# Optimization experiments

Hardware: AMD Instinct MI355X
Metric: run time of the kernel (lower is better)

Reference implementation:

```python
import jax, jax.numpy as jnp
import numpy as np

B, L, DIM, H = 2, 2048, 1024, 16
HD = DIM // H  # 64
EPS = 1e-6
ROPE_THETA = 10000.0


def _rmsnorm(x, scale):
    # mean of squares in float32 as in torch (dtype=torch.float32)
    ms = jnp.mean(jnp.square(x.astype(jnp.float32)), axis=-1, keepdims=True)
    inv = jax.lax.rsqrt(ms + EPS).astype(x.dtype)
    return x * inv * scale.astype(x.dtype)


def _rope_cos_sin(seq_len, head_dim, dtype):
    inv_freq = 1.0 / (ROPE_THETA ** (jnp.arange(0, head_dim, 2, dtype=jnp.float32) / head_dim))
    ang = jnp.arange(seq_len, dtype=jnp.float32)[:, None] * inv_freq[None, :]  # [L, HD/2]
    cos = jnp.cos(ang)[:, None, :].astype(dtype)  # [L,1,HD/2] broadcast over heads
    sin = jnp.sin(ang)[:, None, :].astype(dtype)
    return cos, sin


def _rope_apply(x, cos, sin):
    # x: [B,L,H,HD]; rotate-half formulation
    x1, x2 = jnp.split(x, 2, axis=-1)
    return jnp.concatenate([x1 * cos - x2 * sin, x2 * cos + x1 * sin], axis=-1)


def setup_inputs() -> dict:
    key = jax.random.key(0)
    k1, k2, k3 = jax.random.split(key, 3)
    x = jax.random.normal(k1, (B, L, DIM), dtype=jnp.float32)
    Wqkv = jax.random.normal(k2, (DIM, 3 * DIM), dtype=jnp.float32) * (DIM ** -0.5)
    Wproj = jax.random.normal(k3, (DIM, DIM), dtype=jnp.float32) * (DIM ** -0.5)
    q_scale = jnp.ones((HD,), dtype=jnp.float32)
    k_scale = jnp.ones((HD,), dtype=jnp.float32)
    bproj = jnp.zeros((DIM,), dtype=jnp.float32)
    return {"x": x, "Wqkv": Wqkv, "q_scale": q_scale, "k_scale": k_scale,
            "Wproj": Wproj, "bproj": bproj}


def reference(x, Wqkv, q_scale, k_scale, Wproj, bproj):
    b, l, c = x.shape
    qkv = x @ Wqkv  # [B,L,3*DIM]
    qkv = qkv.reshape(b, l, 3, H, HD)
    q, k, v = qkv[:, :, 0], qkv[:, :, 1], qkv[:, :, 2]  # each [B,L,H,HD]
    q = _rmsnorm(q, q_scale)
    k = _rmsnorm(k, k_scale)
    cos, sin = _rope_cos_sin(l, HD, x.dtype)
    q = _rope_apply(q, cos, sin)
    k = _rope_apply(k, cos, sin)
    scale = HD ** -0.5
    scores = jnp.einsum('blhd,bmhd->bhlm', q, k) * scale  # [B,H,L,L]
    p = jax.nn.softmax(scores, axis=-1)
    o = jnp.einsum('bhlm,bmhd->blhd', p, v).reshape(b, l, c)
    return o @ Wproj + bproj
```

## Files before the change

### kernel.cpp

```cpp
#include <hip/hip_runtime.h>
#include <hip/hip_bf16.h>
#include <cstdint>

#define B_   2
#define L_   2048
#define DIM_ 1024
#define H_   16
#define HD_  64
#define M_   (B_ * L_)
#define N3_  (3 * DIM_)

typedef unsigned short ushort_t;
typedef __bf16 bf16x8 __attribute__((ext_vector_type(8)));
typedef float  f32x4  __attribute__((ext_vector_type(4)));
typedef float  f32x16 __attribute__((ext_vector_type(16)));
typedef unsigned u32x2_t __attribute__((ext_vector_type(2)));

__device__ __forceinline__ unsigned short f2b(float f) {
  return __builtin_bit_cast(unsigned short, (__bf16)f);
}
__device__ __forceinline__ float b2f(unsigned short s) {
  unsigned u = ((unsigned)s) << 16;
  return __builtin_bit_cast(float, u);
}
__device__ __forceinline__ float fmax3(float a, float b, float c) {
  return fmaxf(fmaxf(a, b), c);
}

__device__ __forceinline__ void plswap(unsigned &a, unsigned &b) {
#if defined(__has_builtin) && __has_builtin(__builtin_amdgcn_permlane32_swap)
  u32x2_t r = __builtin_amdgcn_permlane32_swap(a, b, false, false);
  a = r[0]; b = r[1];
#else
  unsigned sa = (unsigned)__shfl_xor((int)a, 32);
  unsigned sb = (unsigned)__shfl_xor((int)b, 32);
  bool hi = (threadIdx.x & 32) != 0;
  unsigned na = hi ? sb : a;
  unsigned nb = hi ? b : sa;
  a = na; b = nb;
#endif
}

typedef const __attribute__((address_space(1))) void* as1cp;
typedef __attribute__((address_space(3))) void* as3p;
__device__ __forceinline__ void gload_lds16(const void* g, void* l) {
  __builtin_amdgcn_global_load_lds((as1cp)g, (as3p)l, 16, 0, 0);
}

__global__ __launch_bounds__(256)
void conv_bf16(const float* __restrict__ in, ushort_t* __restrict__ out, int n4) {
  int i = blockIdx.x * 256 + threadIdx.x;
  if (i >= n4) return;
  float4 v = *(const float4*)&in[(size_t)i * 4];
  ushort4 o;
  o.x = f2b(v.x); o.y = f2b(v.y); o.z = f2b(v.z); o.w = f2b(v.w);
  *(ushort4*)&out[(size_t)i * 4] = o;
}

__global__ __launch_bounds__(256)
void transpose_conv(const float* __restrict__ in, ushort_t* __restrict__ out,
                    int R, int C) {
  __shared__ float tile[64][65];
  const int t = threadIdx.x;
  const int r0 = blockIdx.y * 64, c0 = blockIdx.x * 64;
#pragma unroll
  for (int p = 0; p < 4; ++p) {
    int r = (t >> 4) + p * 16;
    int c = (t & 15) * 4;
    float4 v = *(const float4*)&in[(size_t)(r0 + r) * C + (c0 + c)];
    tile[r][c + 0] = v.x; tile[r][c + 1] = v.y;
    tile[r][c + 2] = v.z; tile[r][c + 3] = v.w;
  }
  __syncthreads();
#pragma unroll
  for (int p = 0; p < 4; ++p) {
    int cc = (t >> 4) + p * 16;
    int r  = (t & 15) * 4;
    ushort4 o;
    o.x = f2b(tile[r + 0][cc]); o.y = f2b(tile[r + 1][cc]);
    o.z = f2b(tile[r + 2][cc]); o.w = f2b(tile[r + 3][cc]);
    *(ushort4*)&out[(size_t)(c0 + cc) * R + (r0 + r)] = o;
  }
}

__global__ __launch_bounds__(256)
void rope_tab(float* __restrict__ cosT, float* __restrict__ sinT) {
  int idx = blockIdx.x * 256 + threadIdx.x;
  int l = idx >> 5, d = idx & 31;
  float inv_freq = expf(-((float)(2 * d) / 64.f) * logf(10000.f));
  float ang = (float)l * inv_freq;
  cosT[idx] = cosf(ang);
  sinT[idx] = sinf(ang);
}

template <int MODE>
__global__ __launch_bounds__(256)
void gemm_bt(const ushort_t* __restrict__ A, const ushort_t* __restrict__ BT,
             void* __restrict__ Cout, ushort_t* __restrict__ vtout,
             const float* __restrict__ bias, int M, int N, int K, int ldc) {
  __shared__ ushort_t As[128 * 32];
  __shared__ ushort_t Bs[128 * 32];
  const int lane = threadIdx.x & 63;
  const int wid  = threadIdx.x >> 6;
  const int wm = wid >> 1, wn = wid & 1;
  const int m0 = blockIdx.y * 128, n0 = blockIdx.x * 128;
  const int ro = lane & 15, kg = lane >> 4;

  f32x4 acc[4][4] = {};

  for (int k0 = 0; k0 < K; k0 += 32) {
    const int cb = wid * 128;
#pragma unroll
    for (int j = 0; j < 2; ++j) {
      int c = cb + j * 64 + lane;
      gload_lds16(A + (size_t)(m0 + (c >> 2)) * K + k0 + (c & 3) * 8,
                  &As[(cb + j * 64) * 8]);
    }
#pragma unroll
    for (int j = 0; j < 2; ++j) {
      int c = cb + j * 64 + lane;
      gload_lds16(BT + (size_t)(n0 + (c >> 2)) * K + k0 + (c & 3) * 8,
                  &Bs[(cb + j * 64) * 8]);
    }
    __syncthreads();
    bf16x8 af[4], bfr[4];
#pragma unroll
    for (int i = 0; i < 4; ++i)
      af[i] = *(const bf16x8*)&As[(wm * 64 + i * 16 + ro) * 32 + kg * 8];
#pragma unroll
    for (int i = 0; i < 4; ++i)
      bfr[i] = *(const bf16x8*)&Bs[(wn * 64 + i * 16 + ro) * 32 + kg * 8];
#pragma unroll
    for (int i = 0; i < 4; ++i)
#pragma unroll
      for (int j = 0; j < 4; ++j)
        acc[i][j] = __builtin_amdgcn_mfma_f32_16x16x32_bf16(af[i], bfr[j],
                                                            acc[i][j], 0, 0, 0);
    __syncthreads();
  }

  if (MODE == 0) {
    if (n0 < 2048) {
#pragma unroll
      for (int i = 0; i < 4; ++i)
#pragma unroll
        for (int r = 0; r < 4; ++r) {
          int row = m0 + wm * 64 + i * 16 + kg * 4 + r;
#pragma unroll
          for (int j = 0; j < 4; ++j) {
            int col = n0 + wn * 64 + j * 16 + ro;
            ((ushort_t*)Cout)[(size_t)row * ldc + col] = f2b(acc[i][j][r]);
          }
        }
    } else {
#pragma unroll
      for (int i = 0; i < 4; ++i) {
        int rowb = m0 + wm * 64 + i * 16 + kg * 4;
        int bb = rowb >> 11, l = rowb & (L_ - 1);
#pragma unroll
        for (int j = 0; j < 4; ++j) {
          int dg = (n0 - 2048) + wn * 64 + j * 16 + ro;
          ushort4 o;
          o.x = f2b(acc[i][j][0]); o.y = f2b(acc[i][j][1]);
          o.z = f2b(acc[i][j][2]); o.w = f2b(acc[i][j][3]);
          *(ushort4*)&vtout[((size_t)bb * DIM_ + dg) * L_ + l] = o;
        }
      }
    }
  } else {
#pragma unroll
    for (int i = 0; i < 4; ++i)
#pragma unroll
      for (int r = 0; r < 4; ++r) {
        int row = m0 + wm * 64 + i * 16 + kg * 4 + r;
#pragma unroll
        for (int j = 0; j < 4; ++j) {
          int col = n0 + wn * 64 + j * 16 + ro;
          ((float*)Cout)[(size_t)row * ldc + col] = acc[i][j][r] + bias[col];
        }
      }
  }
}

__global__ __launch_bounds__(256)
void rmsrope(ushort_t* __restrict__ qk, const float* __restrict__ qs,
             const float* __restrict__ ks, const float* __restrict__ cosT,
             const float* __restrict__ sinT) {
  const int t = blockIdx.x;
  const int l = t & (L_ - 1);
  const int j = threadIdx.x & 15;
  const int h = threadIdx.x >> 4;
  const int dd = (j & 7) * 4;
  float4 cv = *(const float4*)&cosT[l * 32 + dd];
  float4 sv = *(const float4*)&sinT[l * 32 + dd];
  const float sgn = (j < 8) ? -1.f : 1.f;
#pragma unroll
  for (int ic = 0; ic < 2; ++ic) {
    const float qsc = (ic == 0) ? 0.125f * 1.44269504088896341f : 1.f;
    ushort_t* base = qk + (size_t)t * 2048 + ic * DIM_ + h * HD_ + j * 4;
    ushort4 raw = *(const ushort4*)base;
    float x0 = b2f(raw.x), x1 = b2f(raw.y), x2 = b2f(raw.z), x3 = b2f(raw.w);
    float ss = x0 * x0 + x1 * x1 + x2 * x2 + x3 * x3;
    ss += __shfl_xor(ss, 1); ss += __shfl_xor(ss, 2);
    ss += __shfl_xor(ss, 4); ss += __shfl_xor(ss, 8);
    float inv = rsqrtf(ss * (1.f / 64.f) + 1e-6f);
    const float* scp = (ic == 0 ? qs : ks) + j * 4;
    float4 sc = *(const float4*)scp;
    x0 *= inv * sc.x; x1 *= inv * sc.y; x2 *= inv * sc.z; x3 *= inv * sc.w;
    float y0 = __shfl_xor(x0, 8), y1 = __shfl_xor(x1, 8);
    float y2 = __shfl_xor(x2, 8), y3 = __shfl_xor(x3, 8);
    ushort4 o;
    o.x = f2b((x0 * cv.x + sgn * y0 * sv.x) * qsc);
    o.y = f2b((x1 * cv.y + sgn * y1 * sv.y) * qsc);
    o.z = f2b((x2 * cv.z + sgn * y2 * sv.z) * qsc);
    o.w = f2b((x3 * cv.w + sgn * y3 * sv.w) * qsc);
    *(ushort4*)base = o;
  }
}

template <int SPLIT>
__global__ __launch_bounds__(256, 3)
void flash_attn(const ushort_t* __restrict__ qk, const ushort_t* __restrict__ vt,
                ushort_t* __restrict__ O, ushort_t* __restrict__ Opart,
                float* __restrict__ Ml) {
  const int qt = blockIdx.x, h = blockIdx.y;
  const int b  = SPLIT ? (int)(blockIdx.z >> 1) : (int)blockIdx.z;
  const int ks = SPLIT ? (int)(blockIdx.z & 1) : 0;
  const int ktBeg = SPLIT ? ks * (L_ / 128) : 0;
  const int ktEnd = SPLIT ? ktBeg + (L_ / 128) : (L_ / 64);
  const int lane = threadIdx.x & 63, wid = threadIdx.x >> 6;
  const int lq = lane & 31;
  const int hi = lane >> 5;
  const int q0 = qt * 128;
  const size_t tok0 = (size_t)b * L_;
  const ushort_t* qb = qk + tok0 * 2048 + h * HD_;
  const ushort_t* kb = qb + DIM_;
  const ushort_t* vb = vt + ((size_t)b * DIM_ + h * HD_) * L_;

  __shared__ ushort_t Ks[2][4096];
  __shared__ ushort_t Vs[2][4096];

  const int srow0 = wid * 16 + (lane >> 3);
  const int sc    = (lane & 7) ^ (srow0 & 7);
  const ushort_t* kst = kb + (size_t)(ktBeg * 64 + srow0) * 2048 + sc * 8;
  const ushort_t* vst = vb + (size_t)srow0 * L_ + ktBeg * 64 + sc * 8;
  auto STAGE = [&](int bufi) {
    gload_lds16(kst,            &Ks[bufi][wid * 1024]);
    gload_lds16(kst + 8 * 2048, &Ks[bufi][wid * 1024 + 512]);
    gload_lds16(vst,            &Vs[bufi][wid * 1024]);
    gload_lds16(vst + 8 * L_,   &Vs[bufi][wid * 1024 + 512]);
    kst += 64 * 2048;
    vst += 64;
  };

  bf16x8 qf[4];
  {
    const ushort_t* gp = qb + (size_t)(q0 + wid * 32 + lq) * 2048;
#pragma unroll
    for (int s = 0; s < 4; ++s)
      qf[s] = *(const bf16x8*)(gp + s * 16 + hi * 8);
  }

  int chs[4];
#pragma unroll
  for (int s = 0; s < 4; ++s) chs[s] = ((2 * s + hi) ^ (lq & 7)) * 8;

  f32x16 oaccT[2] = {};
  float mrow = 0.f;
  float lrow = 0.f;

  STAGE(0);
  __syncthreads();

  auto TILE = [&](int bi, bool more) {
    if (more) STAGE(bi ^ 1);
    const ushort_t* kb0 = &Ks[bi][lq * 64];
    const ushort_t* vb0 = &Vs[bi][lq * 64];
#pragma unroll
    for (int t = 0; t < 2; ++t) {
      f32x16 st;
#pragma unroll
      for (int i = 0; i < 16; ++i) st[i] = -mrow;
      __builtin_amdgcn_s_setprio(1);
#pragma unroll
      for (int s = 0; s < 4; ++s) {
        bf16x8 kf = *(const bf16x8*)(kb0 + t * 2048 + chs[s]);
        st = __builtin_amdgcn_mfma_f32_32x32x16_bf16(kf, qf[s], st, 0, 0, 0);
      }
      __builtin_amdgcn_s_setprio(0);

      float m1 = fmax3(st[0],  st[1],  st[2]);
      float m2 = fmax3(st[3],  st[4],  st[5]);
      float m3 = fmax3(st[6],  st[7],  st[8]);
      float m4 = fmax3(st[9],  st[10], st[11]);
      float m5 = fmax3(st[12], st[13], st[14]);
      float n1 = fmax3(m1, m2, st[15]);
      float n2 = fmax3(m3, m4, m5);
      float pm = fmaxf(n1, n2);
      pm = fmaxf(pm, __shfl_xor(pm, 32));

      if (__any(pm > 8.f)) {
        float d = fmaxf(pm, 0.f);
        float alpha = __builtin_amdgcn_exp2f(-d);
        mrow += d;
        lrow *= alpha;
#pragma unroll
        for (int dt = 0; dt < 2; ++dt)
#pragma unroll
          for (int r = 0; r < 16; ++r) oaccT[dt][r] *= alpha;
#pragma unroll
        for (int i = 0; i < 16; ++i) st[i] -= d;
      }

      unsigned pk[8];
      float rs0 = 0.f, rs1 = 0.f;
#pragma unroll
      for (int p = 0; p < 8; ++p) {
        float e0 = __builtin_amdgcn_exp2f(st[2 * p]);
        float e1 = __builtin_amdgcn_exp2f(st[2 * p + 1]);
        rs0 += e0; rs1 += e1;
        pk[p] = (unsigned)f2b(e0) | ((unsigned)f2b(e1) << 16);
      }
      lrow += rs0 + rs1;

      __builtin_amdgcn_s_setprio(1);
#pragma unroll
      for (int blk = 0; blk < 2; ++blk) {
        unsigned w0 = pk[4 * blk + 0], w1 = pk[4 * blk + 1];
        unsigned w2 = pk[4 * blk + 2], w3 = pk[4 * blk + 3];
        plswap(w0, w2);
        plswap(w1, w3);
        uint4 bw; bw.x = w0; bw.y = w1; bw.z = w2; bw.w = w3;
        bf16x8 pf = __builtin_bit_cast(bf16x8, bw);
        const int sg = 2 * t + blk;
#pragma unroll
        for (int dt = 0; dt < 2; ++dt) {
          bf16x8 vf = *(const bf16x8*)(vb0 + dt * 2048 + chs[sg]);
          oaccT[dt] = __builtin_amdgcn_mfma_f32_32x32x16_bf16(vf, pf,
                                                              oaccT[dt], 0, 0, 0);
        }
      }
      __builtin_amdgcn_s_setprio(0);
    }
    __syncthreads();
  };

  const int NT = ktEnd - ktBeg;
  for (int it = 0; it < NT; it += 2) {
    TILE(0, it + 1 < NT);
    TILE(1, it + 2 < NT);
  }

  lrow += __shfl_xor(lrow, 32);
  const float linv = 1.f / lrow;
  const int tok = (int)tok0 + q0 + wid * 32 + lq;
  ushort_t* obp = (SPLIT ? Opart + (size_t)ks * M_ * DIM_ : O)
                  + (size_t)tok * DIM_ + h * HD_;
#pragma unroll
  for (int dt = 0; dt < 2; ++dt)
#pragma unroll
    for (int g4 = 0; g4 < 4; ++g4) {
      int d0 = dt * 32 + g4 * 8 + hi * 4;
      ushort4 o4;
      o4.x = f2b(oaccT[dt][4 * g4 + 0] * linv);
      o4.y = f2b(oaccT[dt][4 * g4 + 1] * linv);
      o4.z = f2b(oaccT[dt][4 * g4 + 2] * linv);
      o4.w = f2b(oaccT[dt][4 * g4 + 3] * linv);
      *(ushort4*)(obp + d0) = o4;
    }
  if (SPLIT && hi == 0) {
    float2 ml; ml.x = mrow; ml.y = lrow;
    *(float2*)&Ml[(((size_t)ks * M_ + tok) * H_ + h) * 2] = ml;
  }
}

__global__ __launch_bounds__(256)
void attn_combine(const ushort_t* __restrict__ Opart, const float* __restrict__ Ml,
                  ushort_t* __restrict__ O) {
  int idx = blockIdx.x * 256 + threadIdx.x;
  int c   = idx & 127;
  int tok = idx >> 7;
  int h   = c >> 3;
  float2 ml0 = *(const float2*)&Ml[(((size_t)0 * M_ + tok) * H_ + h) * 2];
  float2 ml1 = *(const float2*)&Ml[(((size_t)1 * M_ + tok) * H_ + h) * 2];
  float mM = fmaxf(ml0.x, ml1.x);
  float w0 = ml0.y * __builtin_amdgcn_exp2f(ml0.x - mM);
  float w1 = ml1.y * __builtin_amdgcn_exp2f(ml1.x - mM);
  float inv = 1.f / (w0 + w1);
  w0 *= inv; w1 *= inv;
  size_t off = (size_t)tok * DIM_ + c * 8;
  uint4 a = *(const uint4*)&Opart[off];
  uint4 d = *(const uint4*)&Opart[(size_t)M_ * DIM_ + off];
  auto mix = [&](unsigned ua, unsigned ud) -> unsigned {
    float a0 = b2f((unsigned short)(ua & 0xffff)), a1 = b2f((unsigned short)(ua >> 16));
    float d0 = b2f((unsigned short)(ud & 0xffff)), d1 = b2f((unsigned short)(ud >> 16));
    unsigned r0 = f2b(a0 * w0 + d0 * w1), r1 = f2b(a1 * w0 + d1 * w1);
    return r0 | (r1 << 16);
  };
  uint4 o;
  o.x = mix(a.x, d.x); o.y = mix(a.y, d.y);
  o.z = mix(a.z, d.z); o.w = mix(a.w, d.w);
  *(uint4*)&O[off] = o;
}

extern "C" void kernel_launch(void* const* d_in, const int* in_sizes, int n_in,
                              void* d_out, int out_size, void* d_ws, size_t ws_size,
                              hipStream_t stream) {
  const float* x     = (const float*)d_in[0];
  const float* Wqkv  = (const float*)d_in[1];
  const float* qs    = (const float*)d_in[2];
  const float* ks    = (const float*)d_in[3];
  const float* Wproj = (const float*)d_in[4];
  const float* bproj = (const float*)d_in[5];
  float* out = (float*)d_out;

  char* ws = (char*)d_ws;
  ushort_t* xb     = (ushort_t*)(ws);
  ushort_t* WqkvT  = (ushort_t*)(ws + (size_t)(8u << 20));
  ushort_t* WprojT = (ushort_t*)(ws + (size_t)(14u << 20));
  ushort_t* qkb    = (ushort_t*)(ws + (size_t)(16u << 20));
  ushort_t* vtb    = (ushort_t*)(ws + (size_t)(32u << 20));
  float*    cosT   = (float*)(ws + (size_t)(40u << 20));
  float*    sinT   = (float*)(ws + (size_t)(40u << 20) + (256u << 10));
  ushort_t* ob     = (ushort_t*)(ws + (size_t)(41u << 20));
  ushort_t* Opart  = (ushort_t*)(ws + (size_t)(49u << 20));
  float*    Ml     = (float*)(ws + (size_t)(65u << 20));

  conv_bf16<<<4096, 256, 0, stream>>>(x, xb, M_ * DIM_ / 4);
  transpose_conv<<<dim3(48, 16), 256, 0, stream>>>(Wqkv, WqkvT, DIM_, N3_);
  transpose_conv<<<dim3(16, 16), 256, 0, stream>>>(Wproj, WprojT, DIM_, DIM_);
  rope_tab<<<256, 256, 0, stream>>>(cosT, sinT);
  gemm_bt<0><<<dim3(24, 32), 256, 0, stream>>>(xb, WqkvT, qkb, vtb, nullptr,
                                               M_, N3_, DIM_, 2048);
  rmsrope<<<4096, 256, 0, stream>>>(qkb, qs, ks, cosT, sinT);
  if (ws_size >= ((size_t)66u << 20)) {
    flash_attn<1><<<dim3(16, 16, 4), 256, 0, stream>>>(qkb, vtb, nullptr,
                                                       Opart, Ml);
    attn_combine<<<2048, 256, 0, stream>>>(Opart, Ml, ob);
  } else {
    flash_attn<0><<<dim3(16, 16, 2), 256, 0, stream>>>(qkb, vtb, ob,
                                                       nullptr, nullptr);
  }
  gemm_bt<1><<<dim3(8, 32), 256, 0, stream>>>(ob, WprojT, out, nullptr, bproj,
                                              M_, DIM_, DIM_, DIM_);
}
```

Before: 152.7 us.

## Merge preprocessing kernels, batch both score tiles, compute row sums via MFMA

The four preprocessing launches (x conversion, two weight transposes, rope table) become one kernel that dispatches on block index, which removes launch overhead and the gaps between launches. In flash attention, both 32-key sub-tiles are now processed together: their score MFMAs are interleaved, the max and rescale check run once per 64 keys, and the exponentials are computed as one batch. The softmax denominator is now accumulated by an MFMA of a ones vector against the probability fragment instead of scalar adds and a cross-lane shuffle. This adds matrix work per tile and raises register pressure, and the row sum is now taken from the bf16-rounded probabilities.

```diff
diff --git a/kernel.cpp b/kernel.cpp
--- a/kernel.cpp
+++ b/kernel.cpp
@@ -48,49 +48,55 @@
 }
 
 __global__ __launch_bounds__(256)
-void conv_bf16(const float* __restrict__ in, ushort_t* __restrict__ out, int n4) {
-  int i = blockIdx.x * 256 + threadIdx.x;
-  if (i >= n4) return;
-  float4 v = *(const float4*)&in[(size_t)i * 4];
-  ushort4 o;
-  o.x = f2b(v.x); o.y = f2b(v.y); o.z = f2b(v.z); o.w = f2b(v.w);
-  *(ushort4*)&out[(size_t)i * 4] = o;
-}
-
-__global__ __launch_bounds__(256)
-void transpose_conv(const float* __restrict__ in, ushort_t* __restrict__ out,
-                    int R, int C) {
+void preproc(const float* __restrict__ x, ushort_t* __restrict__ xb,
+             const float* __restrict__ Wqkv, ushort_t* __restrict__ WqkvT,
+             const float* __restrict__ Wproj, ushort_t* __restrict__ WprojT,
+             float* __restrict__ cosT, float* __restrict__ sinT) {
   __shared__ float tile[64][65];
+  const int blk = blockIdx.x;
   const int t = threadIdx.x;
-  const int r0 = blockIdx.y * 64, c0 = blockIdx.x * 64;
-#pragma unroll
-  for (int p = 0; p < 4; ++p) {
-    int r = (t >> 4) + p * 16;
-    int c = (t & 15) * 4;
-    float4 v = *(const float4*)&in[(size_t)(r0 + r) * C + (c0 + c)];
-    tile[r][c + 0] = v.x; tile[r][c + 1] = v.y;
-    tile[r][c + 2] = v.z; tile[r][c + 3] = v.w;
-  }
-  __syncthreads();
-#pragma unroll
-  for (int p = 0; p < 4; ++p) {
-    int cc = (t >> 4) + p * 16;
-    int r  = (t & 15) * 4;
+  if (blk < 4096) {
+    int i = blk * 256 + t;
+    float4 v = *(const float4*)&x[(size_t)i * 4];
     ushort4 o;
-    o.x = f2b(tile[r + 0][cc]); o.y = f2b(tile[r + 1][cc]);
-    o.z = f2b(tile[r + 2][cc]); o.w = f2b(tile[r + 3][cc]);
-    *(ushort4*)&out[(size_t)(c0 + cc) * R + (r0 + r)] = o;
-  }
-}
-
-__global__ __launch_bounds__(256)
-void rope_tab(float* __restrict__ cosT, float* __restrict__ sinT) {
-  int idx = blockIdx.x * 256 + threadIdx.x;
-  int l = idx >> 5, d = idx & 31;
-  float inv_freq = expf(-((float)(2 * d) / 64.f) * logf(10000.f));
-  float ang = (float)l * inv_freq;
-  cosT[idx] = cosf(ang);
-  sinT[idx] = sinf(ang);
+    o.x = f2b(v.x); o.y = f2b(v.y); o.z = f2b(v.z); o.w = f2b(v.w);
+    *(ushort4*)&xb[(size_t)i * 4] = o;
+  } else if (blk < 5120) {
+    const float* in;
+    ushort_t* out;
+    int C, bi;
+    if (blk < 4864) { in = Wqkv; out = WqkvT; C = 3072; bi = blk - 4096; }
+    else            { in = Wproj; out = WprojT; C = 1024; bi = blk - 4864; }
+    const int nbx = C >> 6;
+    const int bx = bi % nbx, by = bi / nbx;
+    const int r0 = by * 64, c0 = bx * 64;
+    const int R = 1024;
+#pragma unroll
+    for (int p = 0; p < 4; ++p) {
+      int r = (t >> 4) + p * 16;
+      int c = (t & 15) * 4;
+      float4 v = *(const float4*)&in[(size_t)(r0 + r) * C + (c0 + c)];
+      tile[r][c + 0] = v.x; tile[r][c + 1] = v.y;
+      tile[r][c + 2] = v.z; tile[r][c + 3] = v.w;
+    }
+    __syncthreads();
+#pragma unroll
+    for (int p = 0; p < 4; ++p) {
+      int cc = (t >> 4) + p * 16;
+      int r  = (t & 15) * 4;
+      ushort4 o;
+      o.x = f2b(tile[r + 0][cc]); o.y = f2b(tile[r + 1][cc]);
+      o.z = f2b(tile[r + 2][cc]); o.w = f2b(tile[r + 3][cc]);
+      *(ushort4*)&out[(size_t)(c0 + cc) * R + (r0 + r)] = o;
+    }
+  } else {
+    int idx = (blk - 5120) * 256 + t;
+    int l = idx >> 5, d = idx & 31;
+    float inv_freq = expf(-((float)(2 * d) / 64.f) * logf(10000.f));
+    float ang = (float)l * inv_freq;
+    cosT[idx] = cosf(ang);
+    sinT[idx] = sinf(ang);
+  }
 }
 
 template <int MODE>
@@ -261,13 +267,17 @@
       qf[s] = *(const bf16x8*)(gp + s * 16 + hi * 8);
   }
 
+  bf16x8 onesv;
+#pragma unroll
+  for (int i = 0; i < 8; ++i) onesv[i] = (__bf16)1.0f;
+
   int chs[4];
 #pragma unroll
   for (int s = 0; s < 4; ++s) chs[s] = ((2 * s + hi) ^ (lq & 7)) * 8;
 
   f32x16 oaccT[2] = {};
+  f32x16 laccv = {};
   float mrow = 0.f;
-  float lrow = 0.f;
 
   STAGE(0);
   __syncthreads();
@@ -276,63 +286,77 @@
     if (more) STAGE(bi ^ 1);
     const ushort_t* kb0 = &Ks[bi][lq * 64];
     const ushort_t* vb0 = &Vs[bi][lq * 64];
-#pragma unroll
-    for (int t = 0; t < 2; ++t) {
-      f32x16 st;
-#pragma unroll
-      for (int i = 0; i < 16; ++i) st[i] = -mrow;
-      __builtin_amdgcn_s_setprio(1);
-#pragma unroll
-      for (int s = 0; s < 4; ++s) {
-        bf16x8 kf = *(const bf16x8*)(kb0 + t * 2048 + chs[s]);
-        st = __builtin_amdgcn_mfma_f32_32x32x16_bf16(kf, qf[s], st, 0, 0, 0);
-      }
-      __builtin_amdgcn_s_setprio(0);
-
-      float m1 = fmax3(st[0],  st[1],  st[2]);
-      float m2 = fmax3(st[3],  st[4],  st[5]);
-      float m3 = fmax3(st[6],  st[7],  st[8]);
-      float m4 = fmax3(st[9],  st[10], st[11]);
-      float m5 = fmax3(st[12], st[13], st[14]);
-      float n1 = fmax3(m1, m2, st[15]);
-      float n2 = fmax3(m3, m4, m5);
-      float pm = fmaxf(n1, n2);
-      pm = fmaxf(pm, __shfl_xor(pm, 32));
-
-      if (__any(pm > 8.f)) {
-        float d = fmaxf(pm, 0.f);
-        float alpha = __builtin_amdgcn_exp2f(-d);
-        mrow += d;
-        lrow *= alpha;
-#pragma unroll
-        for (int dt = 0; dt < 2; ++dt)
-#pragma unroll
-          for (int r = 0; r < 16; ++r) oaccT[dt][r] *= alpha;
-#pragma unroll
-        for (int i = 0; i < 16; ++i) st[i] -= d;
-      }
-
-      unsigned pk[8];
-      float rs0 = 0.f, rs1 = 0.f;
-#pragma unroll
-      for (int p = 0; p < 8; ++p) {
-        float e0 = __builtin_amdgcn_exp2f(st[2 * p]);
-        float e1 = __builtin_amdgcn_exp2f(st[2 * p + 1]);
-        rs0 += e0; rs1 += e1;
-        pk[p] = (unsigned)f2b(e0) | ((unsigned)f2b(e1) << 16);
-      }
-      lrow += rs0 + rs1;
-
-      __builtin_amdgcn_s_setprio(1);
+
+    f32x16 st0, st1;
+#pragma unroll
+    for (int i = 0; i < 16; ++i) { st0[i] = -mrow; st1[i] = -mrow; }
+    __builtin_amdgcn_s_setprio(1);
+#pragma unroll
+    for (int s = 0; s < 4; ++s) {
+      bf16x8 kf0 = *(const bf16x8*)(kb0 + chs[s]);
+      bf16x8 kf1 = *(const bf16x8*)(kb0 + 2048 + chs[s]);
+      st0 = __builtin_amdgcn_mfma_f32_32x32x16_bf16(kf0, qf[s], st0, 0, 0, 0);
+      st1 = __builtin_amdgcn_mfma_f32_32x32x16_bf16(kf1, qf[s], st1, 0, 0, 0);
+    }
+    __builtin_amdgcn_s_setprio(0);
+
+    float a0 = fmax3(st0[0],  st0[1],  st0[2]);
+    float a1 = fmax3(st0[3],  st0[4],  st0[5]);
+    float a2 = fmax3(st0[6],  st0[7],  st0[8]);
+    float a3 = fmax3(st0[9],  st0[10], st0[11]);
+    float a4 = fmax3(st0[12], st0[13], st0[14]);
+    float a5 = fmax3(st0[15], st1[0],  st1[1]);
+    float a6 = fmax3(st1[2],  st1[3],  st1[4]);
+    float a7 = fmax3(st1[5],  st1[6],  st1[7]);
+    float a8 = fmax3(st1[8],  st1[9],  st1[10]);
+    float a9 = fmax3(st1[11], st1[12], st1[13]);
+    float aa = fmaxf(st1[14], st1[15]);
+    float c0 = fmax3(a0, a1, a2);
+    float c1 = fmax3(a3, a4, a5);
+    float c2 = fmax3(a6, a7, a8);
+    float c3 = fmax3(a9, aa, c0);
+    float pm = fmax3(c1, c2, c3);
+    pm = fmaxf(pm, __shfl_xor(pm, 32));
+
+    if (__any(pm > 8.f)) {
+      float d = fmaxf(pm, 0.f);
+      float alpha = __builtin_amdgcn_exp2f(-d);
+      mrow += d;
+      laccv[0] *= alpha;
+#pragma unroll
+      for (int dt = 0; dt < 2; ++dt)
+#pragma unroll
+        for (int r = 0; r < 16; ++r) oaccT[dt][r] *= alpha;
+#pragma unroll
+      for (int i = 0; i < 16; ++i) { st0[i] -= d; st1[i] -= d; }
+    }
+
+    unsigned pk0[8], pk1[8];
+#pragma unroll
+    for (int p = 0; p < 8; ++p) {
+      float e0 = __builtin_amdgcn_exp2f(st0[2 * p]);
+      float e1 = __builtin_amdgcn_exp2f(st0[2 * p + 1]);
+      pk0[p] = (unsigned)f2b(e0) | ((unsigned)f2b(e1) << 16);
+      float f0 = __builtin_amdgcn_exp2f(st1[2 * p]);
+      float f1 = __builtin_amdgcn_exp2f(st1[2 * p + 1]);
+      pk1[p] = (unsigned)f2b(f0) | ((unsigned)f2b(f1) << 16);
+    }
+
+    __builtin_amdgcn_s_setprio(1);
+#pragma unroll
+    for (int t = 0; t < 2; ++t)
 #pragma unroll
       for (int blk = 0; blk < 2; ++blk) {
-        unsigned w0 = pk[4 * blk + 0], w1 = pk[4 * blk + 1];
-        unsigned w2 = pk[4 * blk + 2], w3 = pk[4 * blk + 3];
+        unsigned w0 = (t == 0) ? pk0[4 * blk + 0] : pk1[4 * blk + 0];
+        unsigned w1 = (t == 0) ? pk0[4 * blk + 1] : pk1[4 * blk + 1];
+        unsigned w2 = (t == 0) ? pk0[4 * blk + 2] : pk1[4 * blk + 2];
+        unsigned w3 = (t == 0) ? pk0[4 * blk + 3] : pk1[4 * blk + 3];
         plswap(w0, w2);
         plswap(w1, w3);
         uint4 bw; bw.x = w0; bw.y = w1; bw.z = w2; bw.w = w3;
         bf16x8 pf = __builtin_bit_cast(bf16x8, bw);
         const int sg = 2 * t + blk;
+        laccv = __builtin_amdgcn_mfma_f32_32x32x16_bf16(onesv, pf, laccv, 0, 0, 0);
 #pragma unroll
         for (int dt = 0; dt < 2; ++dt) {
           bf16x8 vf = *(const bf16x8*)(vb0 + dt * 2048 + chs[sg]);
@@ -340,8 +364,8 @@
                                                               oaccT[dt], 0, 0, 0);
         }
       }
-      __builtin_amdgcn_s_setprio(0);
-    }
+    __builtin_amdgcn_s_setprio(0);
+
     __syncthreads();
   };
 
@@ -351,7 +375,7 @@
     TILE(1, it + 2 < NT);
   }
 
-  lrow += __shfl_xor(lrow, 32);
+  const float lrow = laccv[0];
   const float linv = 1.f / lrow;
   const int tok = (int)tok0 + q0 + wid * 32 + lq;
   ushort_t* obp = (SPLIT ? Opart + (size_t)ks * M_ * DIM_ : O)
@@ -426,10 +450,8 @@
   ushort_t* Opart  = (ushort_t*)(ws + (size_t)(49u << 20));
   float*    Ml     = (float*)(ws + (size_t)(65u << 20));
 
-  conv_bf16<<<4096, 256, 0, stream>>>(x, xb, M_ * DIM_ / 4);
-  transpose_conv<<<dim3(48, 16), 256, 0, stream>>>(Wqkv, WqkvT, DIM_, N3_);
-  transpose_conv<<<dim3(16, 16), 256, 0, stream>>>(Wproj, WprojT, DIM_, DIM_);
-  rope_tab<<<256, 256, 0, stream>>>(cosT, sinT);
+  preproc<<<5376, 256, 0, stream>>>(x, xb, Wqkv, WqkvT, Wproj, WprojT,
+                                    cosT, sinT);
   gemm_bt<0><<<dim3(24, 32), 256, 0, stream>>>(xb, WqkvT, qkb, vtb, nullptr,
                                                M_, N3_, DIM_, 2048);
   rmsrope<<<4096, 256, 0, stream>>>(qkb, qs, ks, cosT, sinT);
```

New measurement: 145.9 us. 1.05x faster.
